# Performance work log

Measured on AMD Instinct MI355X. Metric: run time of the kernel, lower is better.

The kernel has to match this reference:

```python
import jax, jax.numpy as jnp
import numpy as np

B = 2_097_152
IN_DIM = 16
OUT_DIM = 32
N_GROUPS = 4
GROUP = 4


def round_ste(x):
    # torch Round custom Function: round in fwd, identity grad in bwd
    return x + jax.lax.stop_gradient(jnp.round(x) - x)


def sign_ste(x):
    # torch Sign custom Function: sign in fwd, identity grad in bwd
    return x + jax.lax.stop_gradient(jnp.sign(x) - x)


def setup_inputs() -> dict:
    key = jax.random.key(0)
    kx, kw = jax.random.split(key)
    return {
        "x": jax.random.normal(kx, (B, IN_DIM), dtype=jnp.float32),
        "weight": jax.random.normal(kw, (OUT_DIM, IN_DIM), dtype=jnp.float32),
        "scale": jnp.float32(15.0),   # unused in forward (kept for faithfulness)
        "in_max": jnp.float32(0.0),
        "in_min": jnp.float32(10.0),
    }


def reference(x, weight, scale, in_max, in_min):
    w = sign_ste(weight)                      # (O, I) in {-1,0,1}
    w_plus = jax.nn.relu(w)
    w_minus = jax.nn.relu(-w)
    rng = in_max - in_min
    # quantize input to 4-bit levels [0, 15]
    xq = jnp.clip(round_ste((x - in_min) / rng * 15.0), 0.0, 15.0)  # (B, I)
    # bias correction term: (ones * InMin) @ w^T
    bias = (jnp.ones_like(x) * in_min) @ w.T  # (B, O)
    # bit-sliced group GEMMs: 4 groups of K=4, plus/minus weight planes
    xg = xq.reshape(-1, N_GROUPS, GROUP)          # (B, G, K)
    wpg = w_plus.reshape(OUT_DIM, N_GROUPS, GROUP)   # (O, G, K)
    wmg = w_minus.reshape(OUT_DIM, N_GROUPS, GROUP)  # (O, G, K)
    yp = jnp.einsum('bgk,ogk->bgo', xg, wpg)      # (B, G, O)
    ym = jnp.einsum('bgk,ogk->bgo', xg, wmg)      # (B, G, O)
    # per-slice requantization: clip(round(y/15), -4, 4), summed over groups
    terms = (jnp.clip(round_ste(yp / 15.0), -4.0, 4.0)
             + jnp.clip(round_ste(-ym / 15.0), -4.0, 4.0))  # (B, G, O)
    out = terms.sum(axis=1) * rng + bias          # (B, O)
    return out
```

## Files before the change

### kernel.cpp

```cpp
#include <hip/hip_runtime.h>
#include <stdint.h>

#define THREADS 256

#if __has_builtin(__builtin_amdgcn_udot4)
__device__ __forceinline__ uint32_t dot4acc(uint32_t a, uint32_t m, uint32_t c) {
  return __builtin_amdgcn_udot4(a, m, c, false);
}
#else
__device__ __forceinline__ uint32_t dot4acc(uint32_t a, uint32_t m, uint32_t c) {
  uint32_t mf = m;
  mf |= mf << 1;
  mf |= mf << 2;
  mf |= mf << 4;
  uint32_t t = a & mf;
  uint32_t u = (t & 0xFFFFu) + (t >> 16);
  return (u & 0xFFu) + ((u >> 8) & 0xFFu) + c;
}
#endif

__device__ __forceinline__ float quant1(float v, float in_min, float rng) {
  float t = (v - in_min) / rng * 15.0f;
  t = rintf(t);
  t = fmaxf(t, 0.0f);
  t = fminf(t, 15.0f);
  return t;
}

__device__ __forceinline__ uint32_t quant4(float4 v, float in_min, float rng) {
  uint32_t a = (uint32_t)quant1(v.x, in_min, rng);
  uint32_t b = (uint32_t)quant1(v.y, in_min, rng);
  uint32_t c = (uint32_t)quant1(v.z, in_min, rng);
  uint32_t d = (uint32_t)quant1(v.w, in_min, rng);
  return a | (b << 8) | (c << 16) | (d << 24);
}

__global__ __launch_bounds__(THREADS) void quantlinear_kernel(
    const float* __restrict__ x, const float* __restrict__ weight,
    const float* __restrict__ p_in_max, const float* __restrict__ p_in_min,
    float* __restrict__ out, int rows) {
  __shared__ __align__(16) uint4 sh_mp[32];
  __shared__ __align__(16) uint4 sh_mm[32];
  __shared__ float sh_bias[32];
  __shared__ __align__(16) float4 sh_out[THREADS][8];

  const float in_max = p_in_max[0];
  const float in_min = p_in_min[0];
  const float rng = in_max - in_min;

  const int t = threadIdx.x;
  if (t < 128) {
    const int o = t >> 2, g = t & 3;
    float4 w4 = ((const float4*)weight)[o * 4 + g];
    uint32_t mp = (w4.x > 0.f ? 1u : 0u) | ((w4.y > 0.f ? 1u : 0u) << 8) |
                  ((w4.z > 0.f ? 1u : 0u) << 16) | ((w4.w > 0.f ? 1u : 0u) << 24);
    uint32_t mm = (w4.x < 0.f ? 1u : 0u) | ((w4.y < 0.f ? 1u : 0u) << 8) |
                  ((w4.z < 0.f ? 1u : 0u) << 16) | ((w4.w < 0.f ? 1u : 0u) << 24);
    ((uint32_t*)&sh_mp[o])[g] = mp;
    ((uint32_t*)&sh_mm[o])[g] = mm;
  } else if (t < 160) {
    const int o = t - 128;
    int s = 0;
    for (int i = 0; i < 16; ++i) {
      float w = weight[o * 16 + i];
      s += (w > 0.f) ? 1 : ((w < 0.f) ? -1 : 0);
    }
    sh_bias[o] = in_min * (float)s;
  }
  __syncthreads();

  const int row = blockIdx.x * THREADS + t;
  const bool active = row < rows;

  uint32_t Xq[4] = {0u, 0u, 0u, 0u};
  if (active) {
    const float4* __restrict__ xv = (const float4*)x;
    const size_t rb = (size_t)row * 4;
    float4 xr0 = xv[rb + 0];
    float4 xr1 = xv[rb + 1];
    float4 xr2 = xv[rb + 2];
    float4 xr3 = xv[rb + 3];
    Xq[0] = quant4(xr0, in_min, rng);
    Xq[1] = quant4(xr1, in_min, rng);
    Xq[2] = quant4(xr2, in_min, rng);
    Xq[3] = quant4(xr3, in_min, rng);
  }

#pragma unroll
  for (int oo = 0; oo < 8; ++oo) {
    float res[4];
#pragma unroll
    for (int j = 0; j < 4; ++j) {
      const int o = oo * 4 + j;
      const uint4 mp = sh_mp[o];
      const uint4 mm = sh_mm[o];
      int acc = 0;
#pragma unroll
      for (int g = 0; g < 4; ++g) {
        uint32_t yp7 = dot4acc(Xq[g], ((const uint32_t*)&mp)[g], 7u);
        uint32_t ym7 = dot4acc(Xq[g], ((const uint32_t*)&mm)[g], 7u);
        acc += (int)((yp7 * 1093u) >> 14);
        acc -= (int)((ym7 * 1093u) >> 14);
      }
      res[j] = fmaf((float)acc, rng, sh_bias[o]);
    }
    sh_out[t][(oo + t) & 7] = make_float4(res[0], res[1], res[2], res[3]);
  }
  __syncthreads();

  float4* __restrict__ outv = (float4*)out;
  const size_t gbase = (size_t)blockIdx.x * (THREADS * 8);
  const size_t glim = (size_t)rows * 8;
#pragma unroll
  for (int s = 0; s < 8; ++s) {
    const int i = s * THREADS + t;
    const int r = i >> 3, c = i & 7;
    float4 v = sh_out[r][(c + r) & 7];
    const size_t gi = gbase + (size_t)i;
    if (gi < glim) outv[gi] = v;
  }
}

extern "C" void kernel_launch(void* const* d_in, const int* in_sizes, int n_in,
                              void* d_out, int out_size, void* d_ws, size_t ws_size,
                              hipStream_t stream) {
  const float* x = (const float*)d_in[0];
  const float* w = (const float*)d_in[1];
  const float* in_max = (const float*)d_in[3];
  const float* in_min = (const float*)d_in[4];
  float* out = (float*)d_out;

  const int rows = in_sizes[0] / 16;
  const int blocks = (rows + THREADS - 1) / THREADS;
  quantlinear_kernel<<<blocks, THREADS, 0, stream>>>(x, w, in_max, in_min, out,
                                                     rows);
}
```

Before: 363.9 us.

## Stage quantized inputs in LDS and write outputs directly with coalesced stores

Inputs are now loaded in a coalesced pattern, quantized, and stored as packed bytes in shared memory. Each thread then handles a fixed output-column chunk for 8 rows and keeps its weight masks and bias in registers. Outputs go straight to global memory in coalesced float4 stores. This removes the large output staging buffer in shared memory and the second barrier, which should cut LDS size and raise occupancy, at the cost of per-row shared-memory reads of the quantized inputs.

```diff
diff --git a/kernel.cpp b/kernel.cpp
--- a/kernel.cpp
+++ b/kernel.cpp
@@ -2,6 +2,7 @@
 #include <stdint.h>
 
 #define THREADS 256
+#define ROWS_PER_BLOCK 256
 
 #if __has_builtin(__builtin_amdgcn_udot4)
 __device__ __forceinline__ uint32_t dot4acc(uint32_t a, uint32_t m, uint32_t c) {
@@ -41,14 +42,15 @@
     float* __restrict__ out, int rows) {
   __shared__ __align__(16) uint4 sh_mp[32];
   __shared__ __align__(16) uint4 sh_mm[32];
-  __shared__ float sh_bias[32];
-  __shared__ __align__(16) float4 sh_out[THREADS][8];
+  __shared__ __align__(16) float sh_bias[32];
+  __shared__ __align__(16) uint32_t sh_xq[ROWS_PER_BLOCK * 4];
 
   const float in_max = p_in_max[0];
   const float in_min = p_in_min[0];
   const float rng = in_max - in_min;
 
   const int t = threadIdx.x;
+
   if (t < 128) {
     const int o = t >> 2, g = t & 3;
     float4 w4 = ((const float4*)weight)[o * 4 + g];
@@ -67,57 +69,64 @@
     }
     sh_bias[o] = in_min * (float)s;
   }
+
+  const float4* __restrict__ xv = (const float4*)x;
+  const size_t in_base = (size_t)blockIdx.x * (ROWS_PER_BLOCK * 4);
+  const size_t in_lim = (size_t)rows * 4;
+#pragma unroll
+  for (int s = 0; s < 4; ++s) {
+    const int i = s * THREADS + t;
+    const size_t gi = in_base + (size_t)i;
+    if (gi < in_lim) {
+      float4 v = xv[gi];
+      sh_xq[i] = quant4(v, in_min, rng);
+    }
+  }
   __syncthreads();
 
-  const int row = blockIdx.x * THREADS + t;
-  const bool active = row < rows;
+  const int c = t & 7;
 
-  uint32_t Xq[4] = {0u, 0u, 0u, 0u};
-  if (active) {
-    const float4* __restrict__ xv = (const float4*)x;
-    const size_t rb = (size_t)row * 4;
-    float4 xr0 = xv[rb + 0];
-    float4 xr1 = xv[rb + 1];
-    float4 xr2 = xv[rb + 2];
-    float4 xr3 = xv[rb + 3];
-    Xq[0] = quant4(xr0, in_min, rng);
-    Xq[1] = quant4(xr1, in_min, rng);
-    Xq[2] = quant4(xr2, in_min, rng);
-    Xq[3] = quant4(xr3, in_min, rng);
-  }
+  uint4 mp0 = sh_mp[4 * c + 0], mm0 = sh_mm[4 * c + 0];
+  uint4 mp1 = sh_mp[4 * c + 1], mm1 = sh_mm[4 * c + 1];
+  uint4 mp2 = sh_mp[4 * c + 2], mm2 = sh_mm[4 * c + 2];
+  uint4 mp3 = sh_mp[4 * c + 3], mm3 = sh_mm[4 * c + 3];
+  float4 bias4 = ((const float4*)sh_bias)[c];
+
+  float4* __restrict__ outv = (float4*)out;
+  const size_t out_base = (size_t)blockIdx.x * (ROWS_PER_BLOCK * 8);
+  const size_t out_lim = (size_t)rows * 8;
+  const uint4* sh_xq_v = (const uint4*)sh_xq;
 
 #pragma unroll
-  for (int oo = 0; oo < 8; ++oo) {
+  for (int s = 0; s < 8; ++s) {
+    const int r = (t >> 3) + 32 * s;
+    uint4 Xq = sh_xq_v[r];
+
     float res[4];
 #pragma unroll
     for (int j = 0; j < 4; ++j) {
-      const int o = oo * 4 + j;
-      const uint4 mp = sh_mp[o];
-      const uint4 mm = sh_mm[o];
+      const uint4 mp = (j == 0) ? mp0 : (j == 1) ? mp1 : (j == 2) ? mp2 : mp3;
+      const uint4 mm = (j == 0) ? mm0 : (j == 1) ? mm1 : (j == 2) ? mm2 : mm3;
       int acc = 0;
-#pragma unroll
-      for (int g = 0; g < 4; ++g) {
-        uint32_t yp7 = dot4acc(Xq[g], ((const uint32_t*)&mp)[g], 7u);
-        uint32_t ym7 = dot4acc(Xq[g], ((const uint32_t*)&mm)[g], 7u);
-        acc += (int)((yp7 * 1093u) >> 14);
-        acc -= (int)((ym7 * 1093u) >> 14);
+      {
+        uint32_t yp7, ym7;
+        yp7 = dot4acc(Xq.x, mp.x, 7u); ym7 = dot4acc(Xq.x, mm.x, 7u);
+        acc += (int)((yp7 * 1093u) >> 14) - (int)((ym7 * 1093u) >> 14);
+        yp7 = dot4acc(Xq.y, mp.y, 7u); ym7 = dot4acc(Xq.y, mm.y, 7u);
+        acc += (int)((yp7 * 1093u) >> 14) - (int)((ym7 * 1093u) >> 14);
+        yp7 = dot4acc(Xq.z, mp.z, 7u); ym7 = dot4acc(Xq.z, mm.z, 7u);
+        acc += (int)((yp7 * 1093u) >> 14) - (int)((ym7 * 1093u) >> 14);
+        yp7 = dot4acc(Xq.w, mp.w, 7u); ym7 = dot4acc(Xq.w, mm.w, 7u);
+        acc += (int)((yp7 * 1093u) >> 14) - (int)((ym7 * 1093u) >> 14);
       }
-      res[j] = fmaf((float)acc, rng, sh_bias[o]);
+      const float b = (j == 0) ? bias4.x : (j == 1) ? bias4.y
+                     : (j == 2) ? bias4.z : bias4.w;
+      res[j] = fmaf((float)acc, rng, b);
     }
-    sh_out[t][(oo + t) & 7] = make_float4(res[0], res[1], res[2], res[3]);
-  }
-  __syncthreads();
 
-  float4* __restrict__ outv = (float4*)out;
-  const size_t gbase = (size_t)blockIdx.x * (THREADS * 8);
-  const size_t glim = (size_t)rows * 8;
-#pragma unroll
-  for (int s = 0; s < 8; ++s) {
-    const int i = s * THREADS + t;
-    const int r = i >> 3, c = i & 7;
-    float4 v = sh_out[r][(c + r) & 7];
-    const size_t gi = gbase + (size_t)i;
-    if (gi < glim) outv[gi] = v;
+    const size_t gi = out_base + (size_t)(s * THREADS + t);
+    if (gi < out_lim)
+      outv[gi] = make_float4(res[0], res[1], res[2], res[3]);
   }
 }
 
@@ -131,7 +140,7 @@
   float* out = (float*)d_out;
 
   const int rows = in_sizes[0] / 16;
-  const int blocks = (rows + THREADS - 1) / THREADS;
+  const int blocks = (rows + ROWS_PER_BLOCK - 1) / ROWS_PER_BLOCK;
   quantlinear_kernel<<<blocks, THREADS, 0, stream>>>(x, w, in_max, in_min, out,
                                                      rows);
 }
```

Measured after the change: 366.9 us. Within noise of the previous version (+0.8%).
